# Kernel optimization log

Hardware: AMD Instinct MI355X
Metric: run time of the kernel (lower is better)

## Reference

```python
import jax, jax.numpy as jnp
import numpy as np
from jax import lax

B, DKV, L = 2048, 64, 128   # batch, in/out channels (d_k==d_v), seq len (== d_model)
H, DT = 16, 32              # n_head, d_trans
KW, PAD = 13, 6             # conv kernel width / padding
EPS = 1e-3                  # LayerNormalization eps
TEMPER = np.float32(np.sqrt(128.0))  # sqrt(d_model)


def conv1d(x, w, b):
    # x: (B, Cin, L), w: (Cout, Cin, KW) -> (B, Cout, L)
    y = lax.conv_general_dilated(x, w, window_strides=(1,), padding=[(PAD, PAD)],
                                 dimension_numbers=('NCH', 'OIH', 'NCH'))
    return y + b[None, :, None]


def setup_inputs() -> dict:
    key = jax.random.key(0)
    ks = jax.random.split(key, 20)
    n = lambda i, shape, s: jax.random.normal(ks[i], shape, dtype=jnp.float32) * s
    return {
        'q': n(0, (B, DKV, L), 1.0),
        'k': n(1, (B, DKV, L), 1.0),
        'v': n(2, (B, DKV, L), 1.0),
        # conv projections c_q/c_k/c_v: Conv1d(d_k or d_v -> d_trans, kernel 13)
        'cq_w': n(3, (DT, DKV, KW), 0.05), 'cq_b': n(4, (DT,), 0.05),
        'ck_w': n(5, (DT, DKV, KW), 0.05), 'ck_b': n(6, (DT,), 0.05),
        'cv_w': n(7, (DT, DKV, KW), 0.05), 'cv_b': n(8, (DT,), 0.05),
        # per-head projections (n_head, d_model=128, d_trans=32), xavier-ish scale
        'w_qs': n(9, (H, L, DT), 0.08), 'w_ks': n(10, (H, L, DT), 0.08), 'w_vs': n(11, (H, L, DT), 0.08),
        # proj: Linear(n_head*d_trans=512 -> d_model=128)
        'proj_w': n(12, (L, H * DT), 0.05), 'proj_b': n(13, (L,), 0.05),
        # final_conv: Conv1d(d_trans=32 -> d_v=64, kernel 13)
        'fc_w': n(14, (DKV, DT, KW), 0.05), 'fc_b': n(15, (DKV,), 0.05),
        # custom LayerNormalization over last dim (size 128)
        'ln_a': jnp.ones((L,), jnp.float32), 'ln_b': jnp.zeros((L,), jnp.float32),
    }


def reference(q, k, v, cq_w, cq_b, ck_w, ck_b, cv_w, cv_b,
              w_qs, w_ks, w_vs, proj_w, proj_b, fc_w, fc_b, ln_a, ln_b):
    residual = q  # (B, DKV, L)
    qb = conv1d(q, cq_w, cq_b)  # (B, DT, L)
    kb = conv1d(k, ck_w, ck_b)
    vb = conv1d(v, cv_w, cv_b)
    # per-head linear maps along the length-128 axis: (B,DT,L) x (H,L,DT) -> (H,B,DT,DT)
    qh = jnp.einsum('btl,hld->hbtd', qb, w_qs)
    kh = jnp.einsum('btl,hld->hbtd', kb, w_ks)
    vh = jnp.einsum('btl,hld->hbtd', vb, w_vs)
    scores = jnp.einsum('hbqd,hbkd->hbqk', qh, kh) / TEMPER  # (H,B,32,32)
    attn = jax.nn.softmax(scores, axis=-1)  # dropout inactive at eval
    out = jnp.einsum('hbqk,hbkd->hbqd', attn, vh)  # (H,B,32,32)
    # torch.cat(split(...,B,0), -1) concatenates heads along features, head-major
    out = out.transpose(1, 2, 0, 3).reshape(B, DT, H * DT)  # (B,32,512)
    out = out @ proj_w.T + proj_b  # (B,32,128)
    out = conv1d(out, fc_w, fc_b)  # (B,64,128)
    z = out + residual
    # custom LayerNormalization: unbiased std, divide by (std + eps)
    mu = jnp.mean(z, axis=-1, keepdims=True)
    sigma = jnp.sqrt(jnp.sum((z - mu) ** 2, axis=-1, keepdims=True) / (L - 1))
    return (z - mu) / (sigma + EPS) * ln_a + ln_b
```

## Files before the change

### kernel.cpp

```cpp
#include <hip/hip_runtime.h>
#include <math.h>

#define DEV_INLINE __device__ __forceinline__

constexpr int NB = 2048;
constexpr int C  = 64;
constexpr int L  = 128;
constexpr int DT = 32;
constexpr int NH = 16;
constexpr int KW = 13;
constexpr int PADC = 6;
constexpr float LN_EPS = 1e-3f;
constexpr float RTEMPER = 0.08838834764831845f;

using frag_ab = __attribute__((ext_vector_type(8))) short;
using frag_cd = __attribute__((ext_vector_type(4))) float;

union alignas(16) F16x8 { short s[8]; short4 h[2]; frag_ab f; };

DEV_INLINE short f2bf(float x) {
    unsigned u = __float_as_uint(x);
    unsigned r = (u + 0x7FFFu + ((u >> 16) & 1u)) >> 16;
    return (short)r;
}

__global__ __launch_bounds__(256) void k0_prep(
    const float* __restrict__ wqs, const float* __restrict__ wks,
    const float* __restrict__ wvs, const float* __restrict__ pw,
    const float* __restrict__ cqw, const float* __restrict__ ckw,
    const float* __restrict__ cvw, const float* __restrict__ fcw,
    short* __restrict__ wqB, short* __restrict__ wkB, short* __restrict__ wvB,
    short* __restrict__ projB,
    short* __restrict__ cqA, short* __restrict__ ckA, short* __restrict__ cvA,
    short* __restrict__ fcA)
{
    int idx = blockIdx.x * 256 + threadIdx.x;
    if (idx >= 46080) return;
    F16x8 u;
    if (idx < 32768) {
        int arr = idx >> 13;
        int rem = idx & 8191;
        int h   = rem >> 9;
        int f   = (rem >> 6) & 7;
        int ln  = rem & 63;
        if (arr < 3) {
            const float* w = (arr == 0) ? wqs : (arr == 1 ? wks : wvs);
            int kt = f >> 1, nt = f & 1;
            int n = nt * 16 + (ln & 15);
            int kb = kt * 32 + ((ln >> 4) << 3);
            #pragma unroll
            for (int j = 0; j < 8; ++j)
                u.s[j] = f2bf(w[h * 4096 + (kb + j) * 32 + n]);
            short* dst = (arr == 0) ? wqB : (arr == 1 ? wkB : wvB);
            *(F16x8*)(dst + rem * 8) = u;
        } else {
            int m = f * 16 + (ln & 15);
            int db = (ln >> 4) << 3;
            #pragma unroll
            for (int j = 0; j < 8; ++j)
                u.s[j] = f2bf(pw[m * 512 + h * 32 + db + j]);
            *(F16x8*)(projB + rem * 8) = u;
        }
    } else {
        int idx2 = idx - 32768;
        int arr2 = idx2 / 3328;
        int rem2 = idx2 - arr2 * 3328;
        int f  = rem2 >> 6;
        int ln = rem2 & 63;
        int q8 = (ln >> 4) << 3;
        if (arr2 < 3) {
            const float* w = (arr2 == 0) ? cqw : (arr2 == 1 ? ckw : cvw);
            int mt = f & 1, kt = (f >> 1) & 1, kw = f >> 2;
            int m = mt * 16 + (ln & 15);
            int cib = kt * 32 + q8;
            #pragma unroll
            for (int j = 0; j < 8; ++j)
                u.s[j] = f2bf(w[m * (C * KW) + (cib + j) * KW + kw]);
            short* dst = (arr2 == 0) ? cqA : (arr2 == 1 ? ckA : cvA);
            *(F16x8*)(dst + rem2 * 8) = u;
        } else {
            int mt = f & 3, kw = f >> 2;
            int m = mt * 16 + (ln & 15);
            #pragma unroll
            for (int j = 0; j < 8; ++j)
                u.s[j] = f2bf(fcw[m * (DT * KW) + (q8 + j) * KW + kw]);
            *(F16x8*)(fcA + rem2 * 8) = u;
        }
    }
}

__global__ __launch_bounds__(256) void k1_conv(const float* __restrict__ x,
                                               const short* __restrict__ wA,
                                               const float* __restrict__ bias,
                                               short* __restrict__ outF)
{
    __shared__ __align__(16) short xT[140 * 72];
    __shared__ __align__(16) short ot[32 * 136];

    const int b = blockIdx.x, tid = threadIdx.x;
    const int lane = tid & 63, wv = tid >> 6;
    const int q = lane >> 4, nlo = lane & 15;
    const float* xb = x + (size_t)b * (C * L);

    for (int i = tid; i < 4096; i += 256) {
        int cp = i >> 7, l = i & 127;
        float a  = xb[(2 * cp) * 128 + l];
        float c2 = xb[(2 * cp + 1) * 128 + l];
        unsigned pk = (unsigned)(unsigned short)f2bf(a)
                    | ((unsigned)(unsigned short)f2bf(c2) << 16);
        *(unsigned*)&xT[(l + 6) * 72 + 2 * cp] = pk;
    }
    for (int i = tid; i < 768; i += 256) {
        int rr = i >> 6, c = i & 63;
        int r = rr < 6 ? rr : 128 + rr;
        xT[r * 72 + c] = 0;
    }

    frag_cd acc[2][2];
    #pragma unroll
    for (int mt = 0; mt < 2; ++mt) {
        #pragma unroll
        for (int i = 0; i < 4; ++i) {
            float bv = bias[mt * 16 + q * 4 + i];
            acc[mt][0][i] = bv; acc[mt][1][i] = bv;
        }
    }
    __syncthreads();

    const int nb0 = wv * 32 + nlo;
    for (int f = 0; f < 26; ++f) {
        const int kw = f >> 1;
        frag_ab a0 = *(const frag_ab*)(wA + ((f * 2 + 0) * 64 + lane) * 8);
        frag_ab a1 = *(const frag_ab*)(wA + ((f * 2 + 1) * 64 + lane) * 8);
        const short* bp = &xT[(nb0 + kw) * 72 + (f & 1) * 32 + q * 8];
        frag_ab b0 = *(const frag_ab*)bp;
        frag_ab b1 = *(const frag_ab*)(bp + 16 * 72);
        acc[0][0] = __builtin_amdgcn_mfma_f32_16x16x32_bf16(a0, b0, acc[0][0], 0, 0, 0);
        acc[0][1] = __builtin_amdgcn_mfma_f32_16x16x32_bf16(a0, b1, acc[0][1], 0, 0, 0);
        acc[1][0] = __builtin_amdgcn_mfma_f32_16x16x32_bf16(a1, b0, acc[1][0], 0, 0, 0);
        acc[1][1] = __builtin_amdgcn_mfma_f32_16x16x32_bf16(a1, b1, acc[1][1], 0, 0, 0);
    }

    #pragma unroll
    for (int mt = 0; mt < 2; ++mt)
        #pragma unroll
        for (int ntl = 0; ntl < 2; ++ntl) {
            int col = wv * 32 + ntl * 16 + nlo;
            int r0  = mt * 16 + q * 4;
            #pragma unroll
            for (int i = 0; i < 4; ++i)
                ot[(r0 + i) * 136 + col] = f2bf(acc[mt][ntl][i]);
        }
    __syncthreads();
    short* dst = outF + (size_t)b * 4096;
    #pragma unroll
    for (int s = wv; s < 8; s += 4) {
        int mt = s >> 2, kt = s & 3;
        const short* p = &ot[(mt * 16 + nlo) * 136 + kt * 32 + q * 8];
        F16x8 u; u.h[0] = *(const short4*)p; u.h[1] = *(const short4*)(p + 4);
        *(F16x8*)(dst + (s * 64 + lane) * 8) = u;
    }
}

DEV_INLINE frag_ab ld_frag(const short* buf, int rbase, int lane) {
    const short* p = buf + (rbase + (lane & 15)) * 36 + ((lane >> 4) << 3);
    F16x8 u;
    u.h[0] = *(const short4*)p;
    u.h[1] = *(const short4*)(p + 4);
    return u.f;
}
DEV_INLINE void st_cfrag(short* buf, frag_cd c, int mt, int nt, int lane) {
    const int col = nt * 16 + (lane & 15);
    const int r0  = mt * 16 + ((lane >> 4) << 2);
    #pragma unroll
    for (int i = 0; i < 4; ++i) buf[(r0 + i) * 36 + col] = f2bf(c[i]);
}
DEV_INLINE void st_cfragT(short* buf, frag_cd c, int mt, int nt, int lane) {
    const int col = nt * 16 + (lane & 15);
    const int r0  = mt * 16 + ((lane >> 4) << 2);
    #pragma unroll
    for (int i = 0; i < 4; ++i) buf[col * 36 + r0 + i] = f2bf(c[i]);
}

DEV_INLINE void do_proj(const short* aF, const short* bF, short* dst,
                        bool transp, int lane) {
    frag_ab B[8];
    #pragma unroll
    for (int i = 0; i < 8; ++i)
        B[i] = *(const frag_ab*)(bF + (i * 64 + lane) * 8);
    #pragma unroll
    for (int mt = 0; mt < 2; ++mt) {
        frag_ab A[4];
        #pragma unroll
        for (int kt = 0; kt < 4; ++kt)
            A[kt] = *(const frag_ab*)(aF + ((mt * 4 + kt) * 64 + lane) * 8);
        #pragma unroll
        for (int nt = 0; nt < 2; ++nt) {
            frag_cd acc = {0.f, 0.f, 0.f, 0.f};
            #pragma unroll
            for (int kt = 0; kt < 4; ++kt)
                acc = __builtin_amdgcn_mfma_f32_16x16x32_bf16(A[kt], B[kt*2+nt], acc, 0, 0, 0);
            if (transp) st_cfragT(dst, acc, mt, nt, lane);
            else        st_cfrag (dst, acc, mt, nt, lane);
        }
    }
}

__global__ __launch_bounds__(256) void k2_attn(
    const short* __restrict__ qbF, const short* __restrict__ kbF, const short* __restrict__ vbF,
    const short* __restrict__ wqB, const short* __restrict__ wkB, const short* __restrict__ wvB,
    const short* __restrict__ projB, const float* __restrict__ proj_b,
    short* __restrict__ o3T)
{
    __shared__ __align__(16) char smem_raw[24576 + 27648];
    short* qkvA    = (short*)smem_raw;
    short* scratch = (short*)(smem_raw + 24576);
    float* red     = (float*)(smem_raw + 24576);

    const int b = blockIdx.x, tid = threadIdx.x;
    const int lane = tid & 63, wv = tid >> 6;

    for (int g = tid; g < 1536; g += 256) {
        const short* src = (g < 512 ? qbF : (g < 1024 ? kbF : vbF))
                           + (size_t)b * 4096 + (size_t)(g & 511) * 8;
        *(F16x8*)(qkvA + g * 8) = *(const F16x8*)src;
    }
    __syncthreads();

    short* buf0 = scratch + wv * 3456;
    short* buf1 = buf0 + 1152;
    short* buf2 = buf1 + 1152;

    frag_cd oc[2][8];
    #pragma unroll
    for (int mt = 0; mt < 2; ++mt)
        #pragma unroll
        for (int n8 = 0; n8 < 8; ++n8)
            oc[mt][n8] = frag_cd{0.f, 0.f, 0.f, 0.f};

    for (int hi = 0; hi < 4; ++hi) {
        const int h = hi * 4 + wv;
        do_proj(qkvA,        wqB + h * 4096, buf0, false, lane);
        do_proj(qkvA + 4096, wkB + h * 4096, buf1, false, lane);
        do_proj(qkvA + 8192, wvB + h * 4096, buf2, true,  lane);

        frag_ab bk0 = ld_frag(buf1, 0, lane), bk1 = ld_frag(buf1, 16, lane);
        frag_cd S[2][2];
        #pragma unroll
        for (int mt = 0; mt < 2; ++mt) {
            frag_ab aq = ld_frag(buf0, mt * 16, lane);
            frag_cd z = {0.f, 0.f, 0.f, 0.f};
            S[mt][0] = __builtin_amdgcn_mfma_f32_16x16x32_bf16(aq, bk0, z, 0, 0, 0);
            S[mt][1] = __builtin_amdgcn_mfma_f32_16x16x32_bf16(aq, bk1, z, 0, 0, 0);
        }

        #pragma unroll
        for (int mt = 0; mt < 2; ++mt) {
            #pragma unroll
            for (int i = 0; i < 4; ++i) {
                float s0 = S[mt][0][i] * RTEMPER;
                float s1 = S[mt][1][i] * RTEMPER;
                float mx = fmaxf(s0, s1);
                #pragma unroll
                for (int off = 1; off < 16; off <<= 1)
                    mx = fmaxf(mx, __shfl_xor(mx, off, 64));
                float e0 = __expf(s0 - mx), e1 = __expf(s1 - mx);
                float sm = e0 + e1;
                #pragma unroll
                for (int off = 1; off < 16; off <<= 1)
                    sm += __shfl_xor(sm, off, 64);
                const float inv = 1.f / sm;
                const int row = mt * 16 + ((lane >> 4) << 2) + i;
                buf0[row * 36 + (lane & 15)]      = f2bf(e0 * inv);
                buf0[row * 36 + 16 + (lane & 15)] = f2bf(e1 * inv);
            }
        }

        frag_ab bv0 = ld_frag(buf2, 0, lane), bv1 = ld_frag(buf2, 16, lane);
        #pragma unroll
        for (int mt = 0; mt < 2; ++mt) {
            frag_ab ap = ld_frag(buf0, mt * 16, lane);
            frag_cd z = {0.f, 0.f, 0.f, 0.f};
            frag_cd O0 = __builtin_amdgcn_mfma_f32_16x16x32_bf16(ap, bv0, z, 0, 0, 0);
            frag_cd O1 = __builtin_amdgcn_mfma_f32_16x16x32_bf16(ap, bv1, z, 0, 0, 0);
            st_cfrag(buf1, O0, mt, 0, lane);
            st_cfrag(buf1, O1, mt, 1, lane);
        }

        frag_ab ao0 = ld_frag(buf1, 0, lane), ao1 = ld_frag(buf1, 16, lane);
        #pragma unroll
        for (int n8 = 0; n8 < 8; ++n8) {
            frag_ab pb = *(const frag_ab*)(projB + h * 4096 + (n8 * 64 + lane) * 8);
            oc[0][n8] = __builtin_amdgcn_mfma_f32_16x16x32_bf16(ao0, pb, oc[0][n8], 0, 0, 0);
            oc[1][n8] = __builtin_amdgcn_mfma_f32_16x16x32_bf16(ao1, pb, oc[1][n8], 0, 0, 0);
        }
    }

    __syncthreads();
    for (int w = 0; w < 4; ++w) {
        if (wv == w) {
            #pragma unroll
            for (int mt = 0; mt < 2; ++mt)
                #pragma unroll
                for (int n8 = 0; n8 < 8; ++n8)
                    #pragma unroll
                    for (int i = 0; i < 4; ++i) {
                        const int r = mt * 16 + ((lane >> 4) << 2) + i;
                        const int cix = n8 * 16 + (lane & 15);
                        const int ix = r * 128 + cix;
                        const float val = oc[mt][n8][i];
                        red[ix] = (w == 0) ? val : red[ix] + val;
                    }
        }
        __syncthreads();
    }
    short* dst = o3T + (size_t)b * 4096;
    for (int i = tid; i < 4096; i += 256) {
        int l = i >> 5, t = i & 31;
        dst[i] = f2bf(red[t * 128 + l] + proj_b[l]);
    }
}

__global__ __launch_bounds__(256) void k3_fconv_ln(
    const short* __restrict__ o3T,
    const short* __restrict__ fA,
    const float* __restrict__ fcb,
    const float* __restrict__ resid,
    const float* __restrict__ ln_a, const float* __restrict__ ln_b,
    float* __restrict__ out)
{
    __shared__ __align__(16) short xT[140 * 40];
    __shared__ __align__(16) float zb[64 * 132];

    const int b = blockIdx.x, tid = threadIdx.x;
    const int lane = tid & 63, wv = tid >> 6;
    const int q = lane >> 4, nlo = lane & 15;

    const short* src = o3T + (size_t)b * 4096;
    for (int c = tid; c < 512; c += 256) {
        int l = c >> 2, t0 = (c & 3) * 8;
        *(F16x8*)(&xT[(l + 6) * 40 + t0]) = *(const F16x8*)(src + l * 32 + t0);
    }
    for (int i = tid; i < 384; i += 256) {
        int rr = i >> 5, cc = i & 31;
        int r = rr < 6 ? rr : 128 + rr;
        xT[r * 40 + cc] = 0;
    }

    frag_cd acc[4][2];
    #pragma unroll
    for (int mt = 0; mt < 4; ++mt) {
        #pragma unroll
        for (int i = 0; i < 4; ++i) {
            float bv = fcb[mt * 16 + q * 4 + i];
            acc[mt][0][i] = bv; acc[mt][1][i] = bv;
        }
    }
    __syncthreads();

    const int nb0 = wv * 32 + nlo;
    for (int kw = 0; kw < 13; ++kw) {
        frag_ab a[4];
        #pragma unroll
        for (int mt = 0; mt < 4; ++mt)
            a[mt] = *(const frag_ab*)(fA + ((kw * 4 + mt) * 64 + lane) * 8);
        const short* bp = &xT[(nb0 + kw) * 40 + q * 8];
        frag_ab b0 = *(const frag_ab*)bp;
        frag_ab b1 = *(const frag_ab*)(bp + 16 * 40);
        #pragma unroll
        for (int mt = 0; mt < 4; ++mt) {
            acc[mt][0] = __builtin_amdgcn_mfma_f32_16x16x32_bf16(a[mt], b0, acc[mt][0], 0, 0, 0);
            acc[mt][1] = __builtin_amdgcn_mfma_f32_16x16x32_bf16(a[mt], b1, acc[mt][1], 0, 0, 0);
        }
    }

    #pragma unroll
    for (int mt = 0; mt < 4; ++mt)
        #pragma unroll
        for (int ntl = 0; ntl < 2; ++ntl) {
            int col = wv * 32 + ntl * 16 + nlo;
            int r0  = mt * 16 + q * 4;
            #pragma unroll
            for (int i = 0; i < 4; ++i)
                zb[(r0 + i) * 132 + col] = acc[mt][ntl][i];
        }
    __syncthreads();

    const int cq = tid >> 4, lq = tid & 15, l0 = lq * 8;
    const float4* la4 = (const float4*)(ln_a + l0);
    const float4* lb4 = (const float4*)(ln_b + l0);
    float4 A0 = la4[0], A1 = la4[1], B0 = lb4[0], B1 = lb4[1];
    for (int g = 0; g < 4; ++g) {
        const int co = g * 16 + cq;
        const float4* zr4 = (const float4*)(&zb[co * 132 + l0]);
        float4 z0 = zr4[0], z1 = zr4[1];
        const float4* rr4 = (const float4*)(resid + (size_t)b * (C * L) + co * 128 + l0);
        float4 r0 = rr4[0], r1 = rr4[1];
        float zz[8] = {z0.x + r0.x, z0.y + r0.y, z0.z + r0.z, z0.w + r0.w,
                       z1.x + r1.x, z1.y + r1.y, z1.z + r1.z, z1.w + r1.w};
        float s = 0.f;
        #pragma unroll
        for (int j = 0; j < 8; ++j) s += zz[j];
        #pragma unroll
        for (int off = 1; off < 16; off <<= 1) s += __shfl_xor(s, off, 64);
        const float mu = s * (1.f / 128.f);
        float d[8], ss = 0.f;
        #pragma unroll
        for (int j = 0; j < 8; ++j) { d[j] = zz[j] - mu; ss += d[j] * d[j]; }
        #pragma unroll
        for (int off = 1; off < 16; off <<= 1) ss += __shfl_xor(ss, off, 64);
        const float sigma = sqrtf(ss * (1.f / 127.f));
        const float inv = 1.f / (sigma + LN_EPS);
        float4 o0, o1;
        o0.x = fmaf(d[0] * inv, A0.x, B0.x);
        o0.y = fmaf(d[1] * inv, A0.y, B0.y);
        o0.z = fmaf(d[2] * inv, A0.z, B0.z);
        o0.w = fmaf(d[3] * inv, A0.w, B0.w);
        o1.x = fmaf(d[4] * inv, A1.x, B1.x);
        o1.y = fmaf(d[5] * inv, A1.y, B1.y);
        o1.z = fmaf(d[6] * inv, A1.z, B1.z);
        o1.w = fmaf(d[7] * inv, A1.w, B1.w);
        float4* ow = (float4*)(out + (size_t)b * (C * L) + co * 128 + l0);
        ow[0] = o0; ow[1] = o1;
    }
}

extern "C" void kernel_launch(void* const* d_in, const int* in_sizes, int n_in,
                              void* d_out, int out_size, void* d_ws, size_t ws_size,
                              hipStream_t stream) {
    const float* q    = (const float*)d_in[0];
    const float* k    = (const float*)d_in[1];
    const float* v    = (const float*)d_in[2];
    const float* cq_w = (const float*)d_in[3];  const float* cq_b = (const float*)d_in[4];
    const float* ck_w = (const float*)d_in[5];  const float* ck_b = (const float*)d_in[6];
    const float* cv_w = (const float*)d_in[7];  const float* cv_b = (const float*)d_in[8];
    const float* w_qs = (const float*)d_in[9];
    const float* w_ks = (const float*)d_in[10];
    const float* w_vs = (const float*)d_in[11];
    const float* proj_w = (const float*)d_in[12];
    const float* proj_b = (const float*)d_in[13];
    const float* fc_w = (const float*)d_in[14]; const float* fc_b = (const float*)d_in[15];
    const float* ln_a = (const float*)d_in[16]; const float* ln_b = (const float*)d_in[17];
    float* out = (float*)d_out;

    short* ws16 = (short*)d_ws;
    const size_t SZF = (size_t)NB * 4096;
    short* qbF = ws16;
    short* kbF = qbF + SZF;
    short* vbF = kbF + SZF;
    short* o3T = vbF + SZF;
    short* wqB = o3T + SZF;
    short* wkB = wqB + 65536;
    short* wvB = wkB + 65536;
    short* projB = wvB + 65536;
    short* cqA = projB + 65536;
    short* ckA = cqA + 26624;
    short* cvA = ckA + 26624;
    short* fcA = cvA + 26624;

    k0_prep<<<180, 256, 0, stream>>>(w_qs, w_ks, w_vs, proj_w,
                                     cq_w, ck_w, cv_w, fc_w,
                                     wqB, wkB, wvB, projB, cqA, ckA, cvA, fcA);
    k1_conv<<<NB, 256, 0, stream>>>(q, cqA, cq_b, qbF);
    k1_conv<<<NB, 256, 0, stream>>>(k, ckA, ck_b, kbF);
    k1_conv<<<NB, 256, 0, stream>>>(v, cvA, cv_b, vbF);
    k2_attn<<<NB, 256, 0, stream>>>(qbF, kbF, vbF, wqB, wkB, wvB, projB, proj_b, o3T);
    k3_fconv_ln<<<NB, 256, 0, stream>>>(o3T, fcA, fc_b, q, ln_a, ln_b, out);
}
```

Before: 440.2 us.

## Fuse conv projections, attention, output proj, final conv and layernorm into one kernel

Replaces the three input-conv launches, the attention kernel and the final conv/LN kernel with a single per-batch kernel that keeps the bf16 intermediates in shared memory. This removes the global-memory round trips for the qb/kb/vb and o3T workspaces and four kernel launches. The output projection is now split across waves by output column, with a block-wide sync each head round, replacing the cross-wave shared-memory reduction. Input loads are vectorised to float4. Shared memory use and launch_bounds(256,3) may limit occupancy, and the added barriers serialise work within each block.

```diff
diff --git a/kernel.cpp b/kernel.cpp
--- a/kernel.cpp
+++ b/kernel.cpp
@@ -22,6 +22,9 @@
     unsigned u = __float_as_uint(x);
     unsigned r = (u + 0x7FFFu + ((u >> 16) & 1u)) >> 16;
     return (short)r;
+}
+DEV_INLINE unsigned pack2bf(float a, float b) {
+    return (unsigned)(unsigned short)f2bf(a) | ((unsigned)(unsigned short)f2bf(b) << 16);
 }
 
 __global__ __launch_bounds__(256) void k0_prep(
@@ -89,79 +92,6 @@
     }
 }
 
-__global__ __launch_bounds__(256) void k1_conv(const float* __restrict__ x,
-                                               const short* __restrict__ wA,
-                                               const float* __restrict__ bias,
-                                               short* __restrict__ outF)
-{
-    __shared__ __align__(16) short xT[140 * 72];
-    __shared__ __align__(16) short ot[32 * 136];
-
-    const int b = blockIdx.x, tid = threadIdx.x;
-    const int lane = tid & 63, wv = tid >> 6;
-    const int q = lane >> 4, nlo = lane & 15;
-    const float* xb = x + (size_t)b * (C * L);
-
-    for (int i = tid; i < 4096; i += 256) {
-        int cp = i >> 7, l = i & 127;
-        float a  = xb[(2 * cp) * 128 + l];
-        float c2 = xb[(2 * cp + 1) * 128 + l];
-        unsigned pk = (unsigned)(unsigned short)f2bf(a)
-                    | ((unsigned)(unsigned short)f2bf(c2) << 16);
-        *(unsigned*)&xT[(l + 6) * 72 + 2 * cp] = pk;
-    }
-    for (int i = tid; i < 768; i += 256) {
-        int rr = i >> 6, c = i & 63;
-        int r = rr < 6 ? rr : 128 + rr;
-        xT[r * 72 + c] = 0;
-    }
-
-    frag_cd acc[2][2];
-    #pragma unroll
-    for (int mt = 0; mt < 2; ++mt) {
-        #pragma unroll
-        for (int i = 0; i < 4; ++i) {
-            float bv = bias[mt * 16 + q * 4 + i];
-            acc[mt][0][i] = bv; acc[mt][1][i] = bv;
-        }
-    }
-    __syncthreads();
-
-    const int nb0 = wv * 32 + nlo;
-    for (int f = 0; f < 26; ++f) {
-        const int kw = f >> 1;
-        frag_ab a0 = *(const frag_ab*)(wA + ((f * 2 + 0) * 64 + lane) * 8);
-        frag_ab a1 = *(const frag_ab*)(wA + ((f * 2 + 1) * 64 + lane) * 8);
-        const short* bp = &xT[(nb0 + kw) * 72 + (f & 1) * 32 + q * 8];
-        frag_ab b0 = *(const frag_ab*)bp;
-        frag_ab b1 = *(const frag_ab*)(bp + 16 * 72);
-        acc[0][0] = __builtin_amdgcn_mfma_f32_16x16x32_bf16(a0, b0, acc[0][0], 0, 0, 0);
-        acc[0][1] = __builtin_amdgcn_mfma_f32_16x16x32_bf16(a0, b1, acc[0][1], 0, 0, 0);
-        acc[1][0] = __builtin_amdgcn_mfma_f32_16x16x32_bf16(a1, b0, acc[1][0], 0, 0, 0);
-        acc[1][1] = __builtin_amdgcn_mfma_f32_16x16x32_bf16(a1, b1, acc[1][1], 0, 0, 0);
-    }
-
-    #pragma unroll
-    for (int mt = 0; mt < 2; ++mt)
-        #pragma unroll
-        for (int ntl = 0; ntl < 2; ++ntl) {
-            int col = wv * 32 + ntl * 16 + nlo;
-            int r0  = mt * 16 + q * 4;
-            #pragma unroll
-            for (int i = 0; i < 4; ++i)
-                ot[(r0 + i) * 136 + col] = f2bf(acc[mt][ntl][i]);
-        }
-    __syncthreads();
-    short* dst = outF + (size_t)b * 4096;
-    #pragma unroll
-    for (int s = wv; s < 8; s += 4) {
-        int mt = s >> 2, kt = s & 3;
-        const short* p = &ot[(mt * 16 + nlo) * 136 + kt * 32 + q * 8];
-        F16x8 u; u.h[0] = *(const short4*)p; u.h[1] = *(const short4*)(p + 4);
-        *(F16x8*)(dst + (s * 64 + lane) * 8) = u;
-    }
-}
-
 DEV_INLINE frag_ab ld_frag(const short* buf, int rbase, int lane) {
     const short* p = buf + (rbase + (lane & 15)) * 36 + ((lane >> 4) << 3);
     F16x8 u;
@@ -182,8 +112,8 @@
     for (int i = 0; i < 4; ++i) buf[col * 36 + r0 + i] = f2bf(c[i]);
 }
 
-DEV_INLINE void do_proj(const short* aF, const short* bF, short* dst,
-                        bool transp, int lane) {
+DEV_INLINE void proj_head(const short* __restrict__ tile, const short* __restrict__ bF,
+                          short* dst, bool transp, int lane) {
     frag_ab B[8];
     #pragma unroll
     for (int i = 0; i < 8; ++i)
@@ -192,8 +122,11 @@
     for (int mt = 0; mt < 2; ++mt) {
         frag_ab A[4];
         #pragma unroll
-        for (int kt = 0; kt < 4; ++kt)
-            A[kt] = *(const frag_ab*)(aF + ((mt * 4 + kt) * 64 + lane) * 8);
+        for (int kt = 0; kt < 4; ++kt) {
+            const short* p = tile + (mt * 16 + (lane & 15)) * 136 + kt * 32 + ((lane >> 4) << 3);
+            F16x8 u; u.h[0] = *(const short4*)p; u.h[1] = *(const short4*)(p + 4);
+            A[kt] = u.f;
+        }
         #pragma unroll
         for (int nt = 0; nt < 2; ++nt) {
             frag_cd acc = {0.f, 0.f, 0.f, 0.f};
@@ -206,43 +139,104 @@
     }
 }
 
-__global__ __launch_bounds__(256) void k2_attn(
-    const short* __restrict__ qbF, const short* __restrict__ kbF, const short* __restrict__ vbF,
+__global__ __launch_bounds__(256, 3) void k_fused(
+    const float* __restrict__ qx, const float* __restrict__ kx, const float* __restrict__ vx,
+    const short* __restrict__ cqA, const short* __restrict__ ckA, const short* __restrict__ cvA,
+    const float* __restrict__ cqb, const float* __restrict__ ckb, const float* __restrict__ cvb,
     const short* __restrict__ wqB, const short* __restrict__ wkB, const short* __restrict__ wvB,
     const short* __restrict__ projB, const float* __restrict__ proj_b,
-    short* __restrict__ o3T)
+    const short* __restrict__ fA, const float* __restrict__ fcb,
+    const float* __restrict__ ln_a, const float* __restrict__ ln_b,
+    float* __restrict__ out)
 {
-    __shared__ __align__(16) char smem_raw[24576 + 27648];
-    short* qkvA    = (short*)smem_raw;
-    short* scratch = (short*)(smem_raw + 24576);
-    float* red     = (float*)(smem_raw + 24576);
+    __shared__ __align__(16) char smem[53760];
+    short* tiles = (short*)smem;
+    short* regB  = (short*)(smem + 26112);
 
     const int b = blockIdx.x, tid = threadIdx.x;
     const int lane = tid & 63, wv = tid >> 6;
-
-    for (int g = tid; g < 1536; g += 256) {
-        const short* src = (g < 512 ? qbF : (g < 1024 ? kbF : vbF))
-                           + (size_t)b * 4096 + (size_t)(g & 511) * 8;
-        *(F16x8*)(qkvA + g * 8) = *(const F16x8*)src;
-    }
-    __syncthreads();
-
-    short* buf0 = scratch + wv * 3456;
+    const int qq = lane >> 4, nlo = lane & 15;
+    const int nb0 = wv * 32 + nlo;
+
+    {
+        const float* xs[3] = { qx + (size_t)b * 8192, kx + (size_t)b * 8192, vx + (size_t)b * 8192 };
+        const short* was[3] = { cqA, ckA, cvA };
+        const float* bss[3] = { cqb, ckb, cvb };
+        short* xT = regB;
+        #pragma unroll
+        for (int inp = 0; inp < 3; ++inp) {
+            const float* xb = xs[inp];
+            for (int i = tid; i < 1024; i += 256) {
+                int cp = i >> 5, l4 = (i & 31) << 2;
+                float4 a  = *(const float4*)(xb + (2 * cp) * 128 + l4);
+                float4 c2 = *(const float4*)(xb + (2 * cp + 1) * 128 + l4);
+                *(unsigned*)&xT[(l4 + 6) * 72 + 2 * cp] = pack2bf(a.x, c2.x);
+                *(unsigned*)&xT[(l4 + 7) * 72 + 2 * cp] = pack2bf(a.y, c2.y);
+                *(unsigned*)&xT[(l4 + 8) * 72 + 2 * cp] = pack2bf(a.z, c2.z);
+                *(unsigned*)&xT[(l4 + 9) * 72 + 2 * cp] = pack2bf(a.w, c2.w);
+            }
+            for (int i = tid; i < 384; i += 256) {
+                int rr = i >> 5, c2i = (i & 31) * 2;
+                int r = rr < 6 ? rr : 128 + rr;
+                *(unsigned*)&xT[r * 72 + c2i] = 0u;
+            }
+
+            frag_cd acc[2][2];
+            const float* bias = bss[inp];
+            #pragma unroll
+            for (int mt = 0; mt < 2; ++mt)
+                #pragma unroll
+                for (int i = 0; i < 4; ++i) {
+                    float bv = bias[mt * 16 + qq * 4 + i];
+                    acc[mt][0][i] = bv; acc[mt][1][i] = bv;
+                }
+            __syncthreads();
+
+            const short* wA = was[inp];
+            for (int f = 0; f < 26; ++f) {
+                const int kw = f >> 1;
+                frag_ab a0 = *(const frag_ab*)(wA + ((f * 2 + 0) * 64 + lane) * 8);
+                frag_ab a1 = *(const frag_ab*)(wA + ((f * 2 + 1) * 64 + lane) * 8);
+                const short* bp = &xT[(nb0 + kw) * 72 + (f & 1) * 32 + qq * 8];
+                frag_ab b0 = *(const frag_ab*)bp;
+                frag_ab b1 = *(const frag_ab*)(bp + 16 * 72);
+                acc[0][0] = __builtin_amdgcn_mfma_f32_16x16x32_bf16(a0, b0, acc[0][0], 0, 0, 0);
+                acc[0][1] = __builtin_amdgcn_mfma_f32_16x16x32_bf16(a0, b1, acc[0][1], 0, 0, 0);
+                acc[1][0] = __builtin_amdgcn_mfma_f32_16x16x32_bf16(a1, b0, acc[1][0], 0, 0, 0);
+                acc[1][1] = __builtin_amdgcn_mfma_f32_16x16x32_bf16(a1, b1, acc[1][1], 0, 0, 0);
+            }
+
+            short* dstTile = tiles + inp * 4352;
+            #pragma unroll
+            for (int mt = 0; mt < 2; ++mt)
+                #pragma unroll
+                for (int ntl = 0; ntl < 2; ++ntl) {
+                    int col = wv * 32 + ntl * 16 + nlo;
+                    int r0  = mt * 16 + qq * 4;
+                    #pragma unroll
+                    for (int i = 0; i < 4; ++i)
+                        dstTile[(r0 + i) * 136 + col] = f2bf(acc[mt][ntl][i]);
+                }
+            __syncthreads();
+        }
+    }
+
+    short* buf0 = regB + wv * 3456;
     short* buf1 = buf0 + 1152;
     short* buf2 = buf1 + 1152;
 
-    frag_cd oc[2][8];
+    frag_cd oc[2][2];
     #pragma unroll
     for (int mt = 0; mt < 2; ++mt)
         #pragma unroll
-        for (int n8 = 0; n8 < 8; ++n8)
-            oc[mt][n8] = frag_cd{0.f, 0.f, 0.f, 0.f};
-
-    for (int hi = 0; hi < 4; ++hi) {
-        const int h = hi * 4 + wv;
-        do_proj(qkvA,        wqB + h * 4096, buf0, false, lane);
-        do_proj(qkvA + 4096, wkB + h * 4096, buf1, false, lane);
-        do_proj(qkvA + 8192, wvB + h * 4096, buf2, true,  lane);
+        for (int nt = 0; nt < 2; ++nt)
+            oc[mt][nt] = frag_cd{0.f, 0.f, 0.f, 0.f};
+
+    for (int r = 0; r < 4; ++r) {
+        const int h = r * 4 + wv;
+        proj_head(tiles,        wqB + h * 4096, buf0, false, lane);
+        proj_head(tiles + 4352, wkB + h * 4096, buf1, false, lane);
+        proj_head(tiles + 8704, wvB + h * 4096, buf2, true,  lane);
 
         frag_ab bk0 = ld_frag(buf1, 0, lane), bk1 = ld_frag(buf1, 16, lane);
         frag_cd S[2][2];
@@ -286,115 +280,93 @@
             st_cfrag(buf1, O0, mt, 0, lane);
             st_cfrag(buf1, O1, mt, 1, lane);
         }
-
-        frag_ab ao0 = ld_frag(buf1, 0, lane), ao1 = ld_frag(buf1, 16, lane);
-        #pragma unroll
-        for (int n8 = 0; n8 < 8; ++n8) {
-            frag_ab pb = *(const frag_ab*)(projB + h * 4096 + (n8 * 64 + lane) * 8);
-            oc[0][n8] = __builtin_amdgcn_mfma_f32_16x16x32_bf16(ao0, pb, oc[0][n8], 0, 0, 0);
-            oc[1][n8] = __builtin_amdgcn_mfma_f32_16x16x32_bf16(ao1, pb, oc[1][n8], 0, 0, 0);
-        }
-    }
-
-    __syncthreads();
-    for (int w = 0; w < 4; ++w) {
-        if (wv == w) {
-            #pragma unroll
-            for (int mt = 0; mt < 2; ++mt)
-                #pragma unroll
-                for (int n8 = 0; n8 < 8; ++n8)
-                    #pragma unroll
-                    for (int i = 0; i < 4; ++i) {
-                        const int r = mt * 16 + ((lane >> 4) << 2) + i;
-                        const int cix = n8 * 16 + (lane & 15);
-                        const int ix = r * 128 + cix;
-                        const float val = oc[mt][n8][i];
-                        red[ix] = (w == 0) ? val : red[ix] + val;
-                    }
-        }
         __syncthreads();
-    }
-    short* dst = o3T + (size_t)b * 4096;
-    for (int i = tid; i < 4096; i += 256) {
-        int l = i >> 5, t = i & 31;
-        dst[i] = f2bf(red[t * 128 + l] + proj_b[l]);
-    }
-}
-
-__global__ __launch_bounds__(256) void k3_fconv_ln(
-    const short* __restrict__ o3T,
-    const short* __restrict__ fA,
-    const float* __restrict__ fcb,
-    const float* __restrict__ resid,
-    const float* __restrict__ ln_a, const float* __restrict__ ln_b,
-    float* __restrict__ out)
-{
-    __shared__ __align__(16) short xT[140 * 40];
-    __shared__ __align__(16) float zb[64 * 132];
-
-    const int b = blockIdx.x, tid = threadIdx.x;
-    const int lane = tid & 63, wv = tid >> 6;
-    const int q = lane >> 4, nlo = lane & 15;
-
-    const short* src = o3T + (size_t)b * 4096;
-    for (int c = tid; c < 512; c += 256) {
-        int l = c >> 2, t0 = (c & 3) * 8;
-        *(F16x8*)(&xT[(l + 6) * 40 + t0]) = *(const F16x8*)(src + l * 32 + t0);
-    }
+
+        #pragma unroll
+        for (int hh = 0; hh < 4; ++hh) {
+            const short* ob = regB + hh * 3456 + 1152;
+            frag_ab ao0 = ld_frag(ob, 0, lane), ao1 = ld_frag(ob, 16, lane);
+            const int hq = r * 4 + hh;
+            #pragma unroll
+            for (int nt = 0; nt < 2; ++nt) {
+                frag_ab pb = *(const frag_ab*)(projB + hq * 4096 + ((wv * 2 + nt) * 64 + lane) * 8);
+                oc[0][nt] = __builtin_amdgcn_mfma_f32_16x16x32_bf16(ao0, pb, oc[0][nt], 0, 0, 0);
+                oc[1][nt] = __builtin_amdgcn_mfma_f32_16x16x32_bf16(ao1, pb, oc[1][nt], 0, 0, 0);
+            }
+        }
+        __syncthreads();
+    }
+
+    short* xT2 = tiles;
     for (int i = tid; i < 384; i += 256) {
         int rr = i >> 5, cc = i & 31;
-        int r = rr < 6 ? rr : 128 + rr;
-        xT[r * 40 + cc] = 0;
-    }
-
-    frag_cd acc[4][2];
-    #pragma unroll
-    for (int mt = 0; mt < 4; ++mt) {
+        int rw = rr < 6 ? rr : 128 + rr;
+        xT2[rw * 40 + cc] = 0;
+    }
+    {
+        const float pbv0 = proj_b[wv * 32 + (lane & 15)];
+        const float pbv1 = proj_b[wv * 32 + 16 + (lane & 15)];
+        #pragma unroll
+        for (int mt = 0; mt < 2; ++mt)
+            #pragma unroll
+            for (int nt = 0; nt < 2; ++nt) {
+                const int l = wv * 32 + nt * 16 + (lane & 15);
+                const float pbv = nt ? pbv1 : pbv0;
+                #pragma unroll
+                for (int i = 0; i < 4; ++i) {
+                    const int t = mt * 16 + ((lane >> 4) << 2) + i;
+                    xT2[(l + 6) * 40 + t] = f2bf(oc[mt][nt][i] + pbv);
+                }
+            }
+    }
+    __syncthreads();
+
+    frag_cd fa[4][2];
+    #pragma unroll
+    for (int mt = 0; mt < 4; ++mt)
         #pragma unroll
         for (int i = 0; i < 4; ++i) {
-            float bv = fcb[mt * 16 + q * 4 + i];
-            acc[mt][0][i] = bv; acc[mt][1][i] = bv;
-        }
-    }
-    __syncthreads();
-
-    const int nb0 = wv * 32 + nlo;
+            float bv = fcb[mt * 16 + qq * 4 + i];
+            fa[mt][0][i] = bv; fa[mt][1][i] = bv;
+        }
     for (int kw = 0; kw < 13; ++kw) {
         frag_ab a[4];
         #pragma unroll
         for (int mt = 0; mt < 4; ++mt)
             a[mt] = *(const frag_ab*)(fA + ((kw * 4 + mt) * 64 + lane) * 8);
-        const short* bp = &xT[(nb0 + kw) * 40 + q * 8];
+        const short* bp = &xT2[(nb0 + kw) * 40 + qq * 8];
         frag_ab b0 = *(const frag_ab*)bp;
         frag_ab b1 = *(const frag_ab*)(bp + 16 * 40);
         #pragma unroll
         for (int mt = 0; mt < 4; ++mt) {
-            acc[mt][0] = __builtin_amdgcn_mfma_f32_16x16x32_bf16(a[mt], b0, acc[mt][0], 0, 0, 0);
-            acc[mt][1] = __builtin_amdgcn_mfma_f32_16x16x32_bf16(a[mt], b1, acc[mt][1], 0, 0, 0);
-        }
-    }
-
+            fa[mt][0] = __builtin_amdgcn_mfma_f32_16x16x32_bf16(a[mt], b0, fa[mt][0], 0, 0, 0);
+            fa[mt][1] = __builtin_amdgcn_mfma_f32_16x16x32_bf16(a[mt], b1, fa[mt][1], 0, 0, 0);
+        }
+    }
+    __syncthreads();
+
+    float* zb = (float*)smem;
     #pragma unroll
     for (int mt = 0; mt < 4; ++mt)
         #pragma unroll
         for (int ntl = 0; ntl < 2; ++ntl) {
             int col = wv * 32 + ntl * 16 + nlo;
-            int r0  = mt * 16 + q * 4;
+            int r0  = mt * 16 + qq * 4;
             #pragma unroll
             for (int i = 0; i < 4; ++i)
-                zb[(r0 + i) * 132 + col] = acc[mt][ntl][i];
+                zb[(r0 + i) * 132 + col] = fa[mt][ntl][i];
         }
     __syncthreads();
 
-    const int cq = tid >> 4, lq = tid & 15, l0 = lq * 8;
+    const int cq2 = tid >> 4, lq = tid & 15, l0 = lq * 8;
     const float4* la4 = (const float4*)(ln_a + l0);
     const float4* lb4 = (const float4*)(ln_b + l0);
     float4 A0 = la4[0], A1 = la4[1], B0 = lb4[0], B1 = lb4[1];
     for (int g = 0; g < 4; ++g) {
-        const int co = g * 16 + cq;
+        const int co = g * 16 + cq2;
         const float4* zr4 = (const float4*)(&zb[co * 132 + l0]);
         float4 z0 = zr4[0], z1 = zr4[1];
-        const float4* rr4 = (const float4*)(resid + (size_t)b * (C * L) + co * 128 + l0);
+        const float4* rr4 = (const float4*)(qx + (size_t)b * (C * L) + co * 128 + l0);
         float4 r0 = rr4[0], r1 = rr4[1];
         float zz[8] = {z0.x + r0.x, z0.y + r0.y, z0.z + r0.z, z0.w + r0.w,
                        z1.x + r1.x, z1.y + r1.y, z1.z + r1.z, z1.w + r1.w};
@@ -444,12 +416,7 @@
     float* out = (float*)d_out;
 
     short* ws16 = (short*)d_ws;
-    const size_t SZF = (size_t)NB * 4096;
-    short* qbF = ws16;
-    short* kbF = qbF + SZF;
-    short* vbF = kbF + SZF;
-    short* o3T = vbF + SZF;
-    short* wqB = o3T + SZF;
+    short* wqB = ws16;
     short* wkB = wqB + 65536;
     short* wvB = wkB + 65536;
     short* projB = wvB + 65536;
@@ -461,9 +428,7 @@
     k0_prep<<<180, 256, 0, stream>>>(w_qs, w_ks, w_vs, proj_w,
                                      cq_w, ck_w, cv_w, fc_w,
                                      wqB, wkB, wvB, projB, cqA, ckA, cvA, fcA);
-    k1_conv<<<NB, 256, 0, stream>>>(q, cqA, cq_b, qbF);
-    k1_conv<<<NB, 256, 0, stream>>>(k, ckA, ck_b, kbF);
-    k1_conv<<<NB, 256, 0, stream>>>(v, cvA, cv_b, vbF);
-    k2_attn<<<NB, 256, 0, stream>>>(qbF, kbF, vbF, wqB, wkB, wvB, projB, proj_b, o3T);
-    k3_fconv_ln<<<NB, 256, 0, stream>>>(o3T, fcA, fc_b, q, ln_a, ln_b, out);
-}
+    k_fused<<<NB, 256, 0, stream>>>(q, k, v, cqA, ckA, cvA, cq_b, ck_b, cv_b,
+                                    wqB, wkB, wvB, projB, proj_b,
+                                    fcA, fc_b, ln_a, ln_b, out);
+}
```

New measurement: 379.7 us. -13.8%, faster.
